# Performance work log

Hardware: AMD Instinct MI355X
Metric: run time of the kernel (lower is better)

Reference implementation:

```python
import jax, jax.numpy as jnp
import numpy as np

N = 100000   # nodes
E = 25000    # hyperedges
NNZ = 2000000
IN_CH = 64
HEADS = 8
OUT_CH = 8
HO = HEADS * OUT_CH  # 64


def setup_inputs() -> dict:
    key = jax.random.key(0)
    k1, k2, k3, k4, k5 = jax.random.split(key, 5)
    X = jax.random.normal(k1, (N, IN_CH), dtype=jnp.float32)
    vertex = jax.random.randint(k2, (NNZ,), 0, N, dtype=jnp.int64 if jax.config.jax_enable_x64 else jnp.int32)
    edges = jax.random.randint(k3, (NNZ,), 0, E, dtype=jnp.int64 if jax.config.jax_enable_x64 else jnp.int32)
    homo = jax.random.uniform(k4, (E,), dtype=jnp.float32) + 0.1  # positive per-hyperedge scalar
    # nn.Linear(in, heads*out, bias=False): store as [in, heads*out] for X @ W
    W = jax.random.normal(k5, (IN_CH, HO), dtype=jnp.float32) * (1.0 / np.sqrt(IN_CH))
    return {"X": X, "W": W, "homo": homo, "vertex": vertex, "edges": edges}


def reference(X, W, homo, vertex, edges):
    n = X.shape[0]
    e = homo.shape[0]
    Xp = X @ W                                   # [N, H*O]
    Xve = Xp[vertex]                             # [nnz, H*O] gather node->incidence
    # first_aggregate = 'mean': vertex features -> hyperedge features
    Xe_sum = jax.ops.segment_sum(Xve, edges, num_segments=e)
    cnt = jax.ops.segment_sum(jnp.ones((Xve.shape[0],), Xve.dtype), edges, num_segments=e)
    Xe = Xe_sum / jnp.maximum(cnt, 1.0)[:, None]  # [E, H*O]
    Xev = Xe[edges]                              # [nnz, H*O] gather edge->incidence
    he = homo[edges]                             # [nnz]
    att_sum = jax.ops.segment_sum(he, vertex, num_segments=n)[vertex]  # [nnz]
    att = he / att_sum                           # [nnz] (homo > 0 so sums > 0 at incident slots)
    att_Xev = att[:, None] * Xev                 # fused version of att.mm(ones).mul(Xev)
    # second_aggregate = 'sum': hyperedge features -> node features
    Xv = jax.ops.segment_sum(att_Xev, vertex, num_segments=n)  # [N, H*O]
    out = Xp + Xv
    # use_norm: row-l2 normalize with DETACHED norm (scale is a constant wrt grad)
    rownorm = jax.lax.stop_gradient(jnp.linalg.norm(out, axis=1, keepdims=True))
    scale = jnp.where(rownorm > 0, 1.0 / jnp.maximum(rownorm, 1e-30), 0.0)
    return out * scale
```

## Files before the change

### kernel.cpp

```cpp
#include <hip/hip_runtime.h>
#include <hip/hip_bf16.h>


#define SE_LOG 6
#define SV_LOG 8
#define MAXB   2048
#define CH     8192

typedef __attribute__((ext_vector_type(8))) short bf16x8;
typedef __attribute__((ext_vector_type(4))) float f32x4;

__device__ __forceinline__ float bf2f(unsigned short u) {
    union { unsigned int i; float f; } x;
    x.i = ((unsigned int)u) << 16;
    return x.f;
}

__device__ __forceinline__ float bflo(unsigned int u) {
    union { unsigned int i; float f; } x;
    x.i = u << 16;
    return x.f;
}

__device__ __forceinline__ float bfhi(unsigned int u) {
    union { unsigned int i; float f; } x;
    x.i = u & 0xffff0000u;
    return x.f;
}

__device__ __forceinline__ unsigned short f2bf(float f) {
    union { unsigned int i; float ff; } x;
    x.ff = f;
    unsigned int r = x.i + 0x7fff + ((x.i >> 16) & 1);
    return (unsigned short)(r >> 16);
}

__device__ __forceinline__ float loadF(const void* p, size_t i, int bf16mode) {
    return bf16mode ? bf2f(((const unsigned short*)p)[i]) : ((const float*)p)[i];
}

__device__ __forceinline__ int loadI(const void* p, size_t i, int i64mode) {
    return i64mode ? ((const int*)p)[2 * i] : ((const int*)p)[i];
}

__global__ void sniff_kernel(const void* X, const void* vtx, int* flags) {
    if (threadIdx.x != 0 || blockIdx.x != 0) return;
    const unsigned short* u = (const unsigned short*)X;
    int sane = 0;
    for (int i = 0; i < 64; ++i) {
        unsigned short lo = u[2 * i];
        int e = (lo >> 7) & 0xFF;
        if (e >= 110 && e <= 137) ++sane;
    }
    flags[0] = (sane >= 32) ? 1 : 0;
    const int* w = (const int*)vtx;
    int zeros = 0;
    for (int i = 0; i < 64; ++i)
        if (w[2 * i + 1] == 0) ++zeros;
    flags[1] = (zeros >= 32) ? 1 : 0;
}

__global__ void homof_kernel(const void* __restrict__ homo,
                             const int* __restrict__ flags,
                             float* __restrict__ homof, int E) {
    int i = blockIdx.x * blockDim.x + threadIdx.x;
    if (i < E) homof[i] = loadF(homo, i, flags[0]);
}

__global__ __launch_bounds__(256)
void gemm_mfma_kernel(const unsigned short* __restrict__ X,
                      const unsigned short* __restrict__ W,
                      const int* __restrict__ flags,
                      unsigned short* __restrict__ Xpb, int N) {
    if (flags[0] == 0) return;
    __shared__ float Ld[4][16 * 68];
    int tid  = threadIdx.x;
    int lane = tid & 63, w = tid >> 6;
    int quad = lane >> 4, c16 = lane & 15;
    bf16x8 bfrag[4][2];
#pragma unroll
    for (int t = 0; t < 4; ++t)
#pragma unroll
        for (int s = 0; s < 2; ++s)
#pragma unroll
            for (int j = 0; j < 8; ++j)
                bfrag[t][s][j] = (short)W[(s * 32 + quad * 8 + j) * 64 + t * 16 + c16];

    int tiles = (N + 15) >> 4;
    int wid = blockIdx.x * 4 + w;
    int nw  = gridDim.x * 4;
    int lr = lane >> 2, seg = lane & 3;
    for (int tile = wid; tile < tiles; tile += nw) {
        int r0 = tile * 16;
        int rA = r0 + c16; if (rA > N - 1) rA = N - 1;
        bf16x8 a0 = *(const bf16x8*)(X + (size_t)rA * 64 + quad * 8);
        bf16x8 a1 = *(const bf16x8*)(X + (size_t)rA * 64 + 32 + quad * 8);
#pragma unroll
        for (int t = 0; t < 4; ++t) {
            f32x4 z = {0.f, 0.f, 0.f, 0.f};
            z = __builtin_amdgcn_mfma_f32_16x16x32_bf16(a0, bfrag[t][0], z, 0, 0, 0);
            z = __builtin_amdgcn_mfma_f32_16x16x32_bf16(a1, bfrag[t][1], z, 0, 0, 0);
#pragma unroll
            for (int i = 0; i < 4; ++i)
                Ld[w][(quad * 4 + i) * 68 + t * 16 + c16] = z[i];
        }
        int r = r0 + lr;
        if (r < N) {
            const float* src = &Ld[w][lr * 68 + seg * 16];
            unsigned int p[8];
#pragma unroll
            for (int i = 0; i < 8; ++i)
                p[i] = (unsigned)f2bf(src[2 * i]) | ((unsigned)f2bf(src[2 * i + 1]) << 16);
            uint4* dst = (uint4*)(Xpb + (size_t)r * 64 + seg * 16);
            dst[0] = make_uint4(p[0], p[1], p[2], p[3]);
            dst[1] = make_uint4(p[4], p[5], p[6], p[7]);
        }
    }
}

__global__ __launch_bounds__(256)
void gemm_f32_kernel(const void* __restrict__ X, const void* __restrict__ W,
                     const int* __restrict__ flags,
                     unsigned short* __restrict__ Xpb, int N) {
    if (flags[0] == 1) return;
    __shared__ float Ws[64 * 64];
    __shared__ float Xs[16][64];
    int tid = threadIdx.x;
    for (int j = tid; j < 4096; j += 256) Ws[j] = ((const float*)W)[j];
    __syncthreads();
    int lane = tid & 63, w = tid >> 6;
    int wid = (blockIdx.x * 256 + tid) >> 6;
    int nw  = (gridDim.x * 256) >> 6;
    for (int r0 = wid * 4; r0 < N; r0 += nw * 4) {
        if (r0 + 4 <= N) {
            float acc0 = 0.f, acc1 = 0.f, acc2 = 0.f, acc3 = 0.f;
#pragma unroll
            for (int j = 0; j < 4; ++j)
                Xs[w * 4 + j][lane] = ((const float*)X)[(size_t)(r0 + j) * 64 + lane];
#pragma unroll
            for (int k4 = 0; k4 < 16; ++k4) {
                float4 x0 = *(const float4*)&Xs[w * 4 + 0][k4 * 4];
                float4 x1 = *(const float4*)&Xs[w * 4 + 1][k4 * 4];
                float4 x2 = *(const float4*)&Xs[w * 4 + 2][k4 * 4];
                float4 x3 = *(const float4*)&Xs[w * 4 + 3][k4 * 4];
#pragma unroll
                for (int kk = 0; kk < 4; ++kk) {
                    float wv = Ws[(k4 * 4 + kk) * 64 + lane];
                    acc0 = fmaf((&x0.x)[kk], wv, acc0);
                    acc1 = fmaf((&x1.x)[kk], wv, acc1);
                    acc2 = fmaf((&x2.x)[kk], wv, acc2);
                    acc3 = fmaf((&x3.x)[kk], wv, acc3);
                }
            }
            float a[4] = {acc0, acc1, acc2, acc3};
#pragma unroll
            for (int j = 0; j < 4; ++j)
                Xpb[(size_t)(r0 + j) * 64 + lane] = f2bf(a[j]);
        } else {
            for (int r = r0; r < N; ++r) {
                Xs[w * 4][lane] = ((const float*)X)[(size_t)r * 64 + lane];
                float acc = 0.f;
                for (int k = 0; k < 64; ++k)
                    acc = fmaf(Xs[w * 4][k], Ws[k * 64 + lane], acc);
                Xpb[(size_t)r * 64 + lane] = f2bf(acc);
            }
        }
    }
}

__global__ __launch_bounds__(1024)
void bhist_kernel(const void* __restrict__ edges, const void* __restrict__ vertex,
                  const int* __restrict__ flags, int* __restrict__ btot,
                  int* __restrict__ slabc, int sstride,
                  int nnz, int NBE, int NBV, int GC) {
    __shared__ int cnt[MAXB];
    int blk  = blockIdx.x;
    int side = (blk >= GC) ? 1 : 0;
    int b    = side ? blk - GC : blk;
    const void* keys = side ? vertex : edges;
    int sblog = side ? SV_LOG : SE_LOG;
    int nb    = side ? NBV : NBE;
    int bas   = side ? NBE : 0;
    int tid = threadIdx.x;
    for (int j = tid; j < nb; j += 1024) cnt[j] = 0;
    __syncthreads();
    int imode = flags[1];
    int c0 = b * CH, c1 = min(nnz, c0 + CH);
    for (int i = c0 + tid; i < c1; i += 1024)
        atomicAdd(&cnt[loadI(keys, i, imode) >> sblog], 1);
    __syncthreads();
    for (int j = tid; j < nb; j += 1024) {
        int c = cnt[j];
        slabc[(size_t)blk * sstride + j] = c;
        if (c) atomicAdd(&btot[bas + j], c);
    }
}

__global__ void bscan_kernel(const int* __restrict__ btot, int* __restrict__ bbase,
                             int* __restrict__ bcur, int NBT) {
    __shared__ int wsum[16];
    __shared__ int carry_s;
    int tid = threadIdx.x, lane = tid & 63, w = tid >> 6;
    if (tid == 0) carry_s = 0;
    __syncthreads();
    for (int base = 0; base < NBT; base += 1024) {
        int i = base + tid;
        int x = (i < NBT) ? btot[i] : 0;
        int s = x;
#pragma unroll
        for (int d = 1; d < 64; d <<= 1) {
            int t = __shfl_up(s, d, 64);
            if (lane >= d) s += t;
        }
        if (lane == 63) wsum[w] = s;
        __syncthreads();
        if (w == 0 && lane < 16) {
            int v = wsum[lane];
#pragma unroll
            for (int d = 1; d < 16; d <<= 1) {
                int t = __shfl_up(v, d, 64);
                if (lane >= d) v += t;
            }
            wsum[lane] = v;
        }
        __syncthreads();
        int carry = carry_s;
        int excl  = carry + (w > 0 ? wsum[w - 1] : 0) + s - x;
        if (i < NBT) { bbase[i] = excl; bcur[i] = excl; }
        __syncthreads();
        if (tid == 1023) carry_s = carry + wsum[15];
        __syncthreads();
    }
    if (tid == 0) bbase[NBT] = carry_s;
}

__global__ __launch_bounds__(1024)
void bscatter_kernel(const void* __restrict__ edges, const void* __restrict__ vertex,
                     const int* __restrict__ flags, int* __restrict__ bcur,
                     const int* __restrict__ slabc, int sstride,
                     int* __restrict__ buck, int nnz, int NBE, int NBV, int GC,
                     int bitsN, int bitsE) {
    __shared__ int cnt[MAXB];
    __shared__ int gb[MAXB];
    int blk  = blockIdx.x;
    int side = (blk >= GC) ? 1 : 0;
    int b    = side ? blk - GC : blk;
    const void* keys = side ? vertex : edges;
    const void* pay  = side ? edges  : vertex;
    int sblog = side ? SV_LOG : SE_LOG;
    int psh   = side ? bitsE : bitsN;
    int nb    = side ? NBV : NBE;
    int bas   = side ? NBE : 0;
    int tid = threadIdx.x;
    for (int j = tid; j < nb; j += 1024) {
        int c = slabc[(size_t)blk * sstride + j];
        gb[j]  = c ? atomicAdd(&bcur[bas + j], c) : 0;
        cnt[j] = 0;
    }
    __syncthreads();
    int imode = flags[1];
    int c0 = b * CH, c1 = min(nnz, c0 + CH);
    int lmask = (1 << sblog) - 1;
    for (int i = c0 + tid; i < c1; i += 1024) {
        int k   = loadI(keys, i, imode);
        int bkt = k >> sblog;
        int r   = atomicAdd(&cnt[bkt], 1);
        buck[gb[bkt] + r] = ((k & lmask) << psh) | loadI(pay, i, imode);
    }
}

__global__ __launch_bounds__(1024)
void bfinal_kernel(const int* __restrict__ buck, const int* __restrict__ bbase,
                   const float* __restrict__ homof,
                   int* __restrict__ off, int* __restrict__ dest,
                   float* __restrict__ hs,
                   int NBE, int NBV, int E, int N, int bitsN, int bitsE) {
    __shared__ int cnt[1 << SV_LOG];
    __shared__ int sexc[1 << SV_LOG];
    __shared__ float hsum[1 << SV_LOG];
    __shared__ int wsum[16];
    int g    = blockIdx.x;
    int side = (g >= NBE) ? 1 : 0;
    int b    = side ? g - NBE : g;
    int sblog = side ? SV_LOG : SE_LOG;
    int psh   = side ? bitsE : bitsN;
    int pmask = (1 << psh) - 1;
    int nside = side ? N : E;
    int bin0  = b << sblog;
    int nbins = min(1 << sblog, nside - bin0);
    int goff0 = (side ? E : 0) + bin0;
    int s0 = bbase[g], s1 = bbase[g + 1], size = s1 - s0;
    int tid = threadIdx.x, lane = tid & 63, w = tid >> 6;
    for (int j = tid; j < nbins; j += 1024) { cnt[j] = 0; hsum[j] = 0.f; }
    __syncthreads();
    for (int j = tid; j < size; j += 1024)
        atomicAdd(&cnt[buck[s0 + j] >> psh], 1);
    __syncthreads();
    {
        int x = (tid < nbins) ? cnt[tid] : 0;
        int s = x;
#pragma unroll
        for (int d = 1; d < 64; d <<= 1) {
            int t = __shfl_up(s, d, 64);
            if (lane >= d) s += t;
        }
        if (lane == 63) wsum[w] = s;
        __syncthreads();
        if (w == 0 && lane < 16) {
            int v = wsum[lane];
#pragma unroll
            for (int d = 1; d < 16; d <<= 1) {
                int t = __shfl_up(v, d, 64);
                if (lane >= d) v += t;
            }
            wsum[lane] = v;
        }
        __syncthreads();
        int excl = s - x + (w > 0 ? wsum[w - 1] : 0);
        if (tid < nbins) { sexc[tid] = excl; off[goff0 + tid] = s0 + excl; }
    }
    if (side == 1 && b == NBV - 1 && tid == 0) off[E + N] = s1;
    __syncthreads();
    for (int j = tid; j < nbins; j += 1024) cnt[j] = sexc[j];
    __syncthreads();
    if (side == 1) {
        for (int j = tid; j < size; j += 1024) {
            int p  = buck[s0 + j];
            int lb = p >> psh;
            int r  = atomicAdd(&cnt[lb], 1);
            int e  = p & pmask;
            dest[s0 + r] = e;
            atomicAdd(&hsum[lb], homof[e]);
        }
        __syncthreads();
        for (int j = tid; j < nbins; j += 1024) hs[bin0 + j] = hsum[j];
    } else {
        for (int j = tid; j < size; j += 1024) {
            int p = buck[s0 + j];
            int r = atomicAdd(&cnt[p >> psh], 1);
            dest[s0 + r] = p & pmask;
        }
    }
}

__global__ void hist_atomic_kernel(const void* __restrict__ edges,
                                   const void* __restrict__ vertex,
                                   const int* __restrict__ flags,
                                   int* __restrict__ tot, int E, int nnz) {
    int i = blockIdx.x * blockDim.x + threadIdx.x;
    if (i >= nnz) return;
    int imode = flags[1];
    atomicAdd(&tot[loadI(edges, i, imode)], 1);
    atomicAdd(&tot[E + loadI(vertex, i, imode)], 1);
}

__global__ void scan_part_kernel(const int* __restrict__ tot, int* __restrict__ part, int M) {
    int g = blockIdx.x, tid = threadIdx.x;
    int base = g * 2048;
    int sum = 0;
    for (int j = tid; j < 2048; j += 256) {
        int i = base + j;
        sum += (i < M) ? tot[i] : 0;
    }
#pragma unroll
    for (int d = 32; d >= 1; d >>= 1) sum += __shfl_xor(sum, d, 64);
    __shared__ int wsums[4];
    int lane = tid & 63, w = tid >> 6;
    if (lane == 0) wsums[w] = sum;
    __syncthreads();
    if (tid == 0) part[g] = wsums[0] + wsums[1] + wsums[2] + wsums[3];
}

__global__ void scan_root_kernel(int* __restrict__ part, int G,
                                 int* __restrict__ off, int M) {
    int tid = threadIdx.x, lane = tid & 63, w = tid >> 6;
    int x = (tid < G) ? part[tid] : 0;
    int s = x;
#pragma unroll
    for (int d = 1; d < 64; d <<= 1) {
        int t = __shfl_up(s, d, 64);
        if (lane >= d) s += t;
    }
    __shared__ int ws[16];
    if (lane == 63) ws[w] = s;
    __syncthreads();
    if (w == 0 && lane < 16) {
        int v = ws[lane];
#pragma unroll
        for (int d = 1; d < 16; d <<= 1) {
            int t = __shfl_up(v, d, 64);
            if (lane >= d) v += t;
        }
        ws[lane] = v;
    }
    __syncthreads();
    int excl = s - x + (w > 0 ? ws[w - 1] : 0);
    if (tid < G) part[tid] = excl;
    if (tid == 1023) off[M] = ws[15];
}

__global__ void scan_apply_kernel(int* __restrict__ tot, const int* __restrict__ part,
                                  int* __restrict__ off, int M) {
    int g = blockIdx.x, tid = threadIdx.x, lane = tid & 63, w = tid >> 6;
    int base = g * 2048 + tid * 8;
    int e[8]; int s = 0;
#pragma unroll
    for (int j = 0; j < 8; ++j) {
        int i = base + j;
        e[j] = (i < M) ? tot[i] : 0;
        s += e[j];
    }
    int si = s;
#pragma unroll
    for (int d = 1; d < 64; d <<= 1) {
        int t = __shfl_up(si, d, 64);
        if (lane >= d) si += t;
    }
    __shared__ int wsum[4];
    if (lane == 63) wsum[w] = si;
    __syncthreads();
    int wbase = 0;
    for (int ww = 0; ww < w; ++ww) wbase += wsum[ww];
    int run = part[g] + wbase + si - s;
#pragma unroll
    for (int j = 0; j < 8; ++j) {
        int i = base + j;
        if (i < M) off[i] = run;
        run += e[j];
    }
}

__global__ void copy_kernel(const int* __restrict__ src, int* __restrict__ dst, int n) {
    int i = blockIdx.x * blockDim.x + threadIdx.x;
    if (i < n) dst[i] = src[i];
}

__global__ void scatter_atomic_kernel(const void* __restrict__ edges,
                                      const void* __restrict__ vertex,
                                      const int* __restrict__ flags,
                                      int* __restrict__ cur, int* __restrict__ dest,
                                      int E, int nnz) {
    int i = blockIdx.x * blockDim.x + threadIdx.x;
    if (i >= nnz) return;
    int imode = flags[1];
    int e = loadI(edges, i, imode);
    int v = loadI(vertex, i, imode);
    dest[atomicAdd(&cur[e], 1)]     = v;
    dest[atomicAdd(&cur[E + v], 1)] = e;
}

__global__ void hs_fallback_kernel(const int* __restrict__ off,
                                   const int* __restrict__ sorted,
                                   const float* __restrict__ homof,
                                   float* __restrict__ hs, int E, int N) {
    int v = blockIdx.x * blockDim.x + threadIdx.x;
    if (v >= N) return;
    int s = off[E + v], e = off[E + v + 1];
    float t = 0.f;
    for (int j = s; j < e; ++j) t += homof[sorted[j]];
    hs[v] = t;
}

__global__ void edge_mean_kernel(const unsigned short* __restrict__ Xpb,
                                 const int* __restrict__ off,
                                 const int* __restrict__ sorted,
                                 const float* __restrict__ homof,
                                 unsigned short* __restrict__ Ye, int E) {
    int wid  = (blockIdx.x * blockDim.x + threadIdx.x) >> 6;
    int lane = threadIdx.x & 63;
    if (wid >= E) return;
    int g = lane >> 4, c = lane & 15;
    unsigned co = (unsigned)c << 3;
    int start = off[wid], end = off[wid + 1];
    float a0 = 0.f, a1 = 0.f, a2 = 0.f, a3 = 0.f;
    const char* Xb = (const char*)Xpb;
    int j = start + g;
    for (; j + 12 < end; j += 16) {
        int v0 = sorted[j];
        int v1 = sorted[j + 4];
        int v2 = sorted[j + 8];
        int v3 = sorted[j + 12];
        uint2 u0 = *(const uint2*)(Xb + (((unsigned)v0 << 7) + co));
        uint2 u1 = *(const uint2*)(Xb + (((unsigned)v1 << 7) + co));
        uint2 u2 = *(const uint2*)(Xb + (((unsigned)v2 << 7) + co));
        uint2 u3 = *(const uint2*)(Xb + (((unsigned)v3 << 7) + co));
        a0 += (bflo(u0.x) + bflo(u1.x)) + (bflo(u2.x) + bflo(u3.x));
        a1 += (bfhi(u0.x) + bfhi(u1.x)) + (bfhi(u2.x) + bfhi(u3.x));
        a2 += (bflo(u0.y) + bflo(u1.y)) + (bflo(u2.y) + bflo(u3.y));
        a3 += (bfhi(u0.y) + bfhi(u1.y)) + (bfhi(u2.y) + bfhi(u3.y));
    }
    for (; j < end; j += 4) {
        int v = sorted[j];
        uint2 u = *(const uint2*)(Xb + (((unsigned)v << 7) + co));
        a0 += bflo(u.x); a1 += bfhi(u.x);
        a2 += bflo(u.y); a3 += bfhi(u.y);
    }
    a0 += __shfl_xor(a0, 16, 64); a0 += __shfl_xor(a0, 32, 64);
    a1 += __shfl_xor(a1, 16, 64); a1 += __shfl_xor(a1, 32, 64);
    a2 += __shfl_xor(a2, 16, 64); a2 += __shfl_xor(a2, 32, 64);
    a3 += __shfl_xor(a3, 16, 64); a3 += __shfl_xor(a3, 32, 64);
    if (g == 0) {
        float inv = homof[wid] / fmaxf((float)(end - start), 1.f);
        unsigned p0 = (unsigned)f2bf(a0 * inv) | ((unsigned)f2bf(a1 * inv) << 16);
        unsigned p1 = (unsigned)f2bf(a2 * inv) | ((unsigned)f2bf(a3 * inv) << 16);
        *(uint2*)((char*)Ye + (((unsigned)wid << 7) + co)) = make_uint2(p0, p1);
    }
}

__global__ void vertex_out_kernel(const unsigned short* __restrict__ Xpb,
                                  const unsigned short* __restrict__ Ye,
                                  const int* __restrict__ off,
                                  const int* __restrict__ sorted,
                                  const float* __restrict__ hs,
                                  float* __restrict__ out, int E, int N) {
    int wv   = (blockIdx.x * blockDim.x + threadIdx.x) >> 6;
    int lane = threadIdx.x & 63;
    int g = lane >> 3, c = lane & 7;
    int vid = wv * 8 + g;
    if (vid >= N) return;
    unsigned co = (unsigned)c << 4;
    int start = off[E + vid], end = off[E + vid + 1];
    float a0 = 0.f, a1 = 0.f, a2 = 0.f, a3 = 0.f;
    float a4 = 0.f, a5 = 0.f, a6 = 0.f, a7 = 0.f;
    const char* Yb = (const char*)Ye;
    int j = start;
    for (; j + 3 < end; j += 4) {
        int e0 = sorted[j], e1 = sorted[j + 1], e2 = sorted[j + 2], e3 = sorted[j + 3];
        uint4 u0 = *(const uint4*)(Yb + (((unsigned)e0 << 7) + co));
        uint4 u1 = *(const uint4*)(Yb + (((unsigned)e1 << 7) + co));
        uint4 u2 = *(const uint4*)(Yb + (((unsigned)e2 << 7) + co));
        uint4 u3 = *(const uint4*)(Yb + (((unsigned)e3 << 7) + co));
        a0 += (bflo(u0.x) + bflo(u1.x)) + (bflo(u2.x) + bflo(u3.x));
        a1 += (bfhi(u0.x) + bfhi(u1.x)) + (bfhi(u2.x) + bfhi(u3.x));
        a2 += (bflo(u0.y) + bflo(u1.y)) + (bflo(u2.y) + bflo(u3.y));
        a3 += (bfhi(u0.y) + bfhi(u1.y)) + (bfhi(u2.y) + bfhi(u3.y));
        a4 += (bflo(u0.z) + bflo(u1.z)) + (bflo(u2.z) + bflo(u3.z));
        a5 += (bfhi(u0.z) + bfhi(u1.z)) + (bfhi(u2.z) + bfhi(u3.z));
        a6 += (bflo(u0.w) + bflo(u1.w)) + (bflo(u2.w) + bflo(u3.w));
        a7 += (bfhi(u0.w) + bfhi(u1.w)) + (bfhi(u2.w) + bfhi(u3.w));
    }
    for (; j < end; ++j) {
        int e = sorted[j];
        uint4 u = *(const uint4*)(Yb + (((unsigned)e << 7) + co));
        a0 += bflo(u.x); a1 += bfhi(u.x);
        a2 += bflo(u.y); a3 += bfhi(u.y);
        a4 += bflo(u.z); a5 += bfhi(u.z);
        a6 += bflo(u.w); a7 += bfhi(u.w);
    }
    float hsv = hs[vid];
    float inv = (hsv > 0.f) ? 1.f / hsv : 0.f;
    uint4 xu = *(const uint4*)((const char*)Xpb + (((unsigned)vid << 7) + co));
    float r0 = bflo(xu.x) + a0 * inv, r1 = bfhi(xu.x) + a1 * inv;
    float r2 = bflo(xu.y) + a2 * inv, r3 = bfhi(xu.y) + a3 * inv;
    float r4 = bflo(xu.z) + a4 * inv, r5 = bfhi(xu.z) + a5 * inv;
    float r6 = bflo(xu.w) + a6 * inv, r7 = bfhi(xu.w) + a7 * inv;
    float ss = ((r0 * r0 + r1 * r1) + (r2 * r2 + r3 * r3)) +
               ((r4 * r4 + r5 * r5) + (r6 * r6 + r7 * r7));
    ss += __shfl_xor(ss, 1, 64);
    ss += __shfl_xor(ss, 2, 64);
    ss += __shfl_xor(ss, 4, 64);
    float rn    = sqrtf(ss);
    float scale = (rn > 0.f) ? 1.f / fmaxf(rn, 1e-30f) : 0.f;
    char* ob = (char*)out + (((unsigned)vid << 8) + (co << 1));
    *(float4*)ob        = make_float4(r0 * scale, r1 * scale, r2 * scale, r3 * scale);
    *(float4*)(ob + 16) = make_float4(r4 * scale, r5 * scale, r6 * scale, r7 * scale);
}

static inline int ceil_bits(int n) {
    int v = n - 1;
    if (v < 1) v = 1;
    int b = 0;
    while ((1 << b) <= v) ++b;
    return b;
}

extern "C" void kernel_launch(void* const* d_in, const int* in_sizes, int n_in,
                              void* d_out, int out_size, void* d_ws, size_t ws_size,
                              hipStream_t stream) {
    const void* X      = d_in[0];
    const void* W      = d_in[1];
    const void* homo   = d_in[2];
    const void* vertex = d_in[3];
    const void* edges  = d_in[4];
    float* out = (float*)d_out;

    const int N   = in_sizes[0] / 64;
    const int E   = in_sizes[2];
    const int NNZ = in_sizes[3];
    const int M   = E + N;

    const int NBE = (E + (1 << SE_LOG) - 1) >> SE_LOG;
    const int NBV = (N + (1 << SV_LOG) - 1) >> SV_LOG;
    const int NBT = NBE + NBV;
    const int GC  = (NNZ + CH - 1) / CH;
    const int SST = (NBE > NBV ? NBE : NBV);
    const int bitsN = ceil_bits(N);
    const int bitsE = ceil_bits(E);
    const int G   = (M + 2047) / 2048;

    char*  ws = (char*)d_ws;
    size_t o  = 0;
    auto alloc = [&](size_t bytes) -> void* {
        void* p = ws + o;
        o += (bytes + 255) & ~(size_t)255;
        return p;
    };
    int*            flags = (int*)alloc(2 * 4);
    int*            off   = (int*)alloc((size_t)(M + 1) * 4);
    int*            bbase = (int*)alloc((size_t)(NBT + 1) * 4);
    int*            bcur  = (int*)alloc((size_t)NBT * 4);
    int*            btot  = (int*)alloc((size_t)NBT * 4);
    float*          homof = (float*)alloc((size_t)E * 4);
    float*          hs    = (float*)alloc((size_t)N * 4);
    int*            buck  = (int*)alloc((size_t)2 * NNZ * 4);
    int*            sorted= (int*)alloc((size_t)2 * NNZ * 4);
    unsigned short* Xpb   = (unsigned short*)alloc((size_t)N * 64 * 2);
    unsigned short* Ye    = (unsigned short*)alloc((size_t)E * 64 * 2);
    int*            slabc = (int*)alloc((size_t)2 * GC * SST * 4);
    size_t o_common = o;
    bool fast = (o <= ws_size) && NBE <= MAXB && NBV <= MAXB &&
                (SE_LOG + bitsN <= 32) && (SV_LOG + bitsE <= 32) && G <= 1024;
    (void)n_in; (void)out_size;

    sniff_kernel<<<1, 64, 0, stream>>>(X, vertex, flags);
    homof_kernel<<<(E + 255) / 256, 256, 0, stream>>>(homo, flags, homof, E);
    gemm_mfma_kernel<<<1024, 256, 0, stream>>>((const unsigned short*)X,
                                               (const unsigned short*)W,
                                               flags, Xpb, N);
    gemm_f32_kernel<<<512, 256, 0, stream>>>(X, W, flags, Xpb, N);

    if (fast) {
        hipMemsetAsync(btot, 0, (size_t)NBT * 4, stream);
        bhist_kernel<<<2 * GC, 1024, 0, stream>>>(edges, vertex, flags, btot,
                                                  slabc, SST, NNZ, NBE, NBV, GC);
        bscan_kernel<<<1, 1024, 0, stream>>>(btot, bbase, bcur, NBT);
        bscatter_kernel<<<2 * GC, 1024, 0, stream>>>(edges, vertex, flags, bcur,
                                                     slabc, SST, buck, NNZ,
                                                     NBE, NBV, GC, bitsN, bitsE);
        bfinal_kernel<<<NBT, 1024, 0, stream>>>(buck, bbase, homof, off, sorted,
                                                hs, NBE, NBV, E, N, bitsN, bitsE);
    } else {
        o = o_common;
        int* tot  = (int*)alloc((size_t)M * 4);
        int* part = (int*)alloc((size_t)(G + 1) * 4);
        int* cur  = (int*)alloc((size_t)M * 4);
        hipMemsetAsync(tot, 0, (size_t)M * 4, stream);
        int nb = (NNZ + 255) / 256;
        hist_atomic_kernel<<<nb, 256, 0, stream>>>(edges, vertex, flags, tot, E, NNZ);
        scan_part_kernel<<<G, 256, 0, stream>>>(tot, part, M);
        scan_root_kernel<<<1, 1024, 0, stream>>>(part, G, off, M);
        scan_apply_kernel<<<G, 256, 0, stream>>>(tot, part, off, M);
        copy_kernel<<<(M + 255) / 256, 256, 0, stream>>>(off, cur, M);
        scatter_atomic_kernel<<<nb, 256, 0, stream>>>(edges, vertex, flags, cur, sorted, E, NNZ);
        hs_fallback_kernel<<<(N + 255) / 256, 256, 0, stream>>>(off, sorted, homof, hs, E, N);
    }

    edge_mean_kernel<<<(E + 3) / 4, 256, 0, stream>>>(Xpb, off, sorted, homof, Ye, E);
    int vwaves  = (N + 7) / 8;
    int vblocks = (vwaves * 64 + 255) / 256;
    vertex_out_kernel<<<vblocks, 256, 0, stream>>>(Xpb, Ye, off, sorted,
                                                   hs, out, E, N);
}
```

Before: 254.0 us.

## Fuse bucket finalize with edge-mean and vertex-output aggregation using LDS lists

Histogram and scatter now handle both the edge and vertex sides in a single pass over the inputs, so edges and vertex are each read once instead of twice. The per-bucket finalize is merged with the edge-mean and vertex-output computations: the sorted neighbour lists are kept in LDS, and the global sorted array and offset array are no longer written out and read back. A spill path to global memory covers buckets larger than the LDS capacity. In exchange, the fused blocks use a lot of shared memory, which lowers occupancy, and each bucket is handled by a single block, which lowers parallelism in the gather phases.

New measurement: 245.7 us. 1.03x faster.

```diff
diff --git a/kernel.cpp b/kernel.cpp
--- a/kernel.cpp
+++ b/kernel.cpp
@@ -4,8 +4,8 @@
 
 #define SE_LOG 6
 #define SV_LOG 8
-#define MAXB   2048
-#define CH     8192
+#define CH     4096
+#define CAPB   12288
 
 typedef __attribute__((ext_vector_type(8))) short bf16x8;
 typedef __attribute__((ext_vector_type(4))) float f32x4;
@@ -169,30 +169,26 @@
 }
 
 __global__ __launch_bounds__(1024)
-void bhist_kernel(const void* __restrict__ edges, const void* __restrict__ vertex,
-                  const int* __restrict__ flags, int* __restrict__ btot,
-                  int* __restrict__ slabc, int sstride,
-                  int nnz, int NBE, int NBV, int GC) {
-    __shared__ int cnt[MAXB];
-    int blk  = blockIdx.x;
-    int side = (blk >= GC) ? 1 : 0;
-    int b    = side ? blk - GC : blk;
-    const void* keys = side ? vertex : edges;
-    int sblog = side ? SV_LOG : SE_LOG;
-    int nb    = side ? NBV : NBE;
-    int bas   = side ? NBE : 0;
-    int tid = threadIdx.x;
-    for (int j = tid; j < nb; j += 1024) cnt[j] = 0;
+void bhist2_kernel(const void* __restrict__ edges, const void* __restrict__ vertex,
+                   const int* __restrict__ flags, int* __restrict__ btot,
+                   int* __restrict__ slabc, int nnz, int NBE, int NBT) {
+    __shared__ int cnt[2048];
+    int tid = threadIdx.x, b = blockIdx.x;
+    for (int j = tid; j < NBT; j += 1024) cnt[j] = 0;
     __syncthreads();
     int imode = flags[1];
     int c0 = b * CH, c1 = min(nnz, c0 + CH);
-    for (int i = c0 + tid; i < c1; i += 1024)
-        atomicAdd(&cnt[loadI(keys, i, imode) >> sblog], 1);
-    __syncthreads();
-    for (int j = tid; j < nb; j += 1024) {
+    for (int i = c0 + tid; i < c1; i += 1024) {
+        int e = loadI(edges, i, imode);
+        int v = loadI(vertex, i, imode);
+        atomicAdd(&cnt[e >> SE_LOG], 1);
+        atomicAdd(&cnt[NBE + (v >> SV_LOG)], 1);
+    }
+    __syncthreads();
+    for (int j = tid; j < NBT; j += 1024) {
         int c = cnt[j];
-        slabc[(size_t)blk * sstride + j] = c;
-        if (c) atomicAdd(&btot[bas + j], c);
+        slabc[(size_t)b * NBT + j] = c;
+        if (c) atomicAdd(&btot[j], c);
     }
 }
 
@@ -235,66 +231,152 @@
 }
 
 __global__ __launch_bounds__(1024)
-void bscatter_kernel(const void* __restrict__ edges, const void* __restrict__ vertex,
-                     const int* __restrict__ flags, int* __restrict__ bcur,
-                     const int* __restrict__ slabc, int sstride,
-                     int* __restrict__ buck, int nnz, int NBE, int NBV, int GC,
-                     int bitsN, int bitsE) {
-    __shared__ int cnt[MAXB];
-    __shared__ int gb[MAXB];
-    int blk  = blockIdx.x;
-    int side = (blk >= GC) ? 1 : 0;
-    int b    = side ? blk - GC : blk;
-    const void* keys = side ? vertex : edges;
-    const void* pay  = side ? edges  : vertex;
-    int sblog = side ? SV_LOG : SE_LOG;
-    int psh   = side ? bitsE : bitsN;
-    int nb    = side ? NBV : NBE;
-    int bas   = side ? NBE : 0;
-    int tid = threadIdx.x;
-    for (int j = tid; j < nb; j += 1024) {
-        int c = slabc[(size_t)blk * sstride + j];
-        gb[j]  = c ? atomicAdd(&bcur[bas + j], c) : 0;
+void bscatter2_kernel(const void* __restrict__ edges, const void* __restrict__ vertex,
+                      const int* __restrict__ flags, int* __restrict__ bcur,
+                      const int* __restrict__ slabc, int* __restrict__ buck,
+                      int nnz, int NBE, int NBT, int bitsN, int bitsE) {
+    __shared__ int cnt[2048];
+    __shared__ int gb[2048];
+    int tid = threadIdx.x, b = blockIdx.x;
+    for (int j = tid; j < NBT; j += 1024) {
+        int c = slabc[(size_t)b * NBT + j];
+        gb[j]  = c ? atomicAdd(&bcur[j], c) : 0;
         cnt[j] = 0;
     }
     __syncthreads();
     int imode = flags[1];
     int c0 = b * CH, c1 = min(nnz, c0 + CH);
-    int lmask = (1 << sblog) - 1;
     for (int i = c0 + tid; i < c1; i += 1024) {
-        int k   = loadI(keys, i, imode);
-        int bkt = k >> sblog;
-        int r   = atomicAdd(&cnt[bkt], 1);
-        buck[gb[bkt] + r] = ((k & lmask) << psh) | loadI(pay, i, imode);
+        int e = loadI(edges, i, imode);
+        int v = loadI(vertex, i, imode);
+        int be = e >> SE_LOG;
+        int r  = atomicAdd(&cnt[be], 1);
+        buck[gb[be] + r] = ((e & ((1 << SE_LOG) - 1)) << bitsN) | v;
+        int bv = NBE + (v >> SV_LOG);
+        int r2 = atomicAdd(&cnt[bv], 1);
+        buck[gb[bv] + r2] = ((v & ((1 << SV_LOG) - 1)) << bitsE) | e;
     }
 }
 
 __global__ __launch_bounds__(1024)
-void bfinal_kernel(const int* __restrict__ buck, const int* __restrict__ bbase,
-                   const float* __restrict__ homof,
-                   int* __restrict__ off, int* __restrict__ dest,
-                   float* __restrict__ hs,
-                   int NBE, int NBV, int E, int N, int bitsN, int bitsE) {
+void bfe_kernel(const int* __restrict__ buck, const int* __restrict__ bbase,
+                const float* __restrict__ homof, int* __restrict__ spill,
+                const unsigned short* __restrict__ Xpb,
+                unsigned short* __restrict__ Ye, int E, int bitsN) {
+    __shared__ int list[CAPB];
+    __shared__ int cnt[1 << SE_LOG];
+    __shared__ int sexc[1 << SE_LOG];
+    __shared__ int wsum[16];
+    int g = blockIdx.x;
+    int bin0 = g << SE_LOG;
+    int nbins = min(1 << SE_LOG, E - bin0);
+    int s0 = bbase[g], s1 = bbase[g + 1], size = s1 - s0;
+    int tid = threadIdx.x, lane = tid & 63, w = tid >> 6;
+    bool sp = (size > CAPB);
+    int pmask = (1 << bitsN) - 1;
+    for (int j = tid; j < nbins; j += 1024) cnt[j] = 0;
+    __syncthreads();
+    for (int j = tid; j < size; j += 1024)
+        atomicAdd(&cnt[buck[s0 + j] >> bitsN], 1);
+    __syncthreads();
+    {
+        int x = (tid < nbins) ? cnt[tid] : 0;
+        int s = x;
+#pragma unroll
+        for (int d = 1; d < 64; d <<= 1) {
+            int t = __shfl_up(s, d, 64);
+            if (lane >= d) s += t;
+        }
+        if (lane == 63) wsum[w] = s;
+        __syncthreads();
+        if (w == 0 && lane < 16) {
+            int v = wsum[lane];
+#pragma unroll
+            for (int d = 1; d < 16; d <<= 1) {
+                int t = __shfl_up(v, d, 64);
+                if (lane >= d) v += t;
+            }
+            wsum[lane] = v;
+        }
+        __syncthreads();
+        int excl = s - x + (w > 0 ? wsum[w - 1] : 0);
+        if (tid < nbins) sexc[tid] = excl;
+    }
+    __syncthreads();
+    if (tid < nbins) cnt[tid] = sexc[tid];
+    __syncthreads();
+    for (int j = tid; j < size; j += 1024) {
+        int p  = buck[s0 + j];
+        int lb = p >> bitsN;
+        int r  = atomicAdd(&cnt[lb], 1);
+        int v  = p & pmask;
+        if (sp) spill[s0 + r] = v; else list[r] = v;
+    }
+    __syncthreads();
+    int grp = (w << 2) | (lane >> 4);
+    int c = lane & 15;
+    unsigned co = (unsigned)c << 3;
+    if (grp < nbins) {
+        int start = sexc[grp], end = cnt[grp];
+        const char* Xb = (const char*)Xpb;
+        float a0 = 0.f, a1 = 0.f, a2 = 0.f, a3 = 0.f;
+        int j = start;
+        if (!sp) {
+            for (; j + 3 < end; j += 4) {
+                int v0 = list[j], v1 = list[j + 1], v2 = list[j + 2], v3 = list[j + 3];
+                uint2 u0 = *(const uint2*)(Xb + (((unsigned)v0 << 7) + co));
+                uint2 u1 = *(const uint2*)(Xb + (((unsigned)v1 << 7) + co));
+                uint2 u2 = *(const uint2*)(Xb + (((unsigned)v2 << 7) + co));
+                uint2 u3 = *(const uint2*)(Xb + (((unsigned)v3 << 7) + co));
+                a0 += (bflo(u0.x) + bflo(u1.x)) + (bflo(u2.x) + bflo(u3.x));
+                a1 += (bfhi(u0.x) + bfhi(u1.x)) + (bfhi(u2.x) + bfhi(u3.x));
+                a2 += (bflo(u0.y) + bflo(u1.y)) + (bflo(u2.y) + bflo(u3.y));
+                a3 += (bfhi(u0.y) + bfhi(u1.y)) + (bfhi(u2.y) + bfhi(u3.y));
+            }
+            for (; j < end; ++j) {
+                int v = list[j];
+                uint2 u = *(const uint2*)(Xb + (((unsigned)v << 7) + co));
+                a0 += bflo(u.x); a1 += bfhi(u.x);
+                a2 += bflo(u.y); a3 += bfhi(u.y);
+            }
+        } else {
+            for (; j < end; ++j) {
+                int v = spill[s0 + j];
+                uint2 u = *(const uint2*)(Xb + (((unsigned)v << 7) + co));
+                a0 += bflo(u.x); a1 += bfhi(u.x);
+                a2 += bflo(u.y); a3 += bfhi(u.y);
+            }
+        }
+        int e = bin0 + grp;
+        float inv = homof[e] / fmaxf((float)(end - start), 1.f);
+        unsigned p0 = (unsigned)f2bf(a0 * inv) | ((unsigned)f2bf(a1 * inv) << 16);
+        unsigned p1 = (unsigned)f2bf(a2 * inv) | ((unsigned)f2bf(a3 * inv) << 16);
+        *(uint2*)((char*)Ye + (((unsigned)e << 7) + co)) = make_uint2(p0, p1);
+    }
+}
+
+__global__ __launch_bounds__(1024)
+void bfv_kernel(const int* __restrict__ buck, const int* __restrict__ bbase,
+                const float* __restrict__ homof, int* __restrict__ spill,
+                const unsigned short* __restrict__ Xpb,
+                const unsigned short* __restrict__ Ye,
+                float* __restrict__ out, int N, int NBE, int bitsE) {
+    __shared__ int list[CAPB];
     __shared__ int cnt[1 << SV_LOG];
     __shared__ int sexc[1 << SV_LOG];
     __shared__ float hsum[1 << SV_LOG];
     __shared__ int wsum[16];
-    int g    = blockIdx.x;
-    int side = (g >= NBE) ? 1 : 0;
-    int b    = side ? g - NBE : g;
-    int sblog = side ? SV_LOG : SE_LOG;
-    int psh   = side ? bitsE : bitsN;
-    int pmask = (1 << psh) - 1;
-    int nside = side ? N : E;
-    int bin0  = b << sblog;
-    int nbins = min(1 << sblog, nside - bin0);
-    int goff0 = (side ? E : 0) + bin0;
-    int s0 = bbase[g], s1 = bbase[g + 1], size = s1 - s0;
+    int bv = blockIdx.x;
+    int bin0 = bv << SV_LOG;
+    int nbins = min(1 << SV_LOG, N - bin0);
+    int s0 = bbase[NBE + bv], s1 = bbase[NBE + bv + 1], size = s1 - s0;
     int tid = threadIdx.x, lane = tid & 63, w = tid >> 6;
+    bool sp = (size > CAPB);
+    int pmask = (1 << bitsE) - 1;
     for (int j = tid; j < nbins; j += 1024) { cnt[j] = 0; hsum[j] = 0.f; }
     __syncthreads();
     for (int j = tid; j < size; j += 1024)
-        atomicAdd(&cnt[buck[s0 + j] >> psh], 1);
+        atomicAdd(&cnt[buck[s0 + j] >> bitsE], 1);
     __syncthreads();
     {
         int x = (tid < nbins) ? cnt[tid] : 0;
@@ -317,29 +399,81 @@
         }
         __syncthreads();
         int excl = s - x + (w > 0 ? wsum[w - 1] : 0);
-        if (tid < nbins) { sexc[tid] = excl; off[goff0 + tid] = s0 + excl; }
-    }
-    if (side == 1 && b == NBV - 1 && tid == 0) off[E + N] = s1;
-    __syncthreads();
-    for (int j = tid; j < nbins; j += 1024) cnt[j] = sexc[j];
-    __syncthreads();
-    if (side == 1) {
-        for (int j = tid; j < size; j += 1024) {
-            int p  = buck[s0 + j];
-            int lb = p >> psh;
-            int r  = atomicAdd(&cnt[lb], 1);
-            int e  = p & pmask;
-            dest[s0 + r] = e;
-            atomicAdd(&hsum[lb], homof[e]);
-        }
-        __syncthreads();
-        for (int j = tid; j < nbins; j += 1024) hs[bin0 + j] = hsum[j];
-    } else {
-        for (int j = tid; j < size; j += 1024) {
-            int p = buck[s0 + j];
-            int r = atomicAdd(&cnt[p >> psh], 1);
-            dest[s0 + r] = p & pmask;
-        }
+        if (tid < nbins) sexc[tid] = excl;
+    }
+    __syncthreads();
+    if (tid < nbins) cnt[tid] = sexc[tid];
+    __syncthreads();
+    for (int j = tid; j < size; j += 1024) {
+        int p  = buck[s0 + j];
+        int lb = p >> bitsE;
+        int r  = atomicAdd(&cnt[lb], 1);
+        int e  = p & pmask;
+        if (sp) spill[s0 + r] = e; else list[r] = e;
+        atomicAdd(&hsum[lb], homof[e]);
+    }
+    __syncthreads();
+    int grp = (w << 3) | (lane >> 3);
+    int c = lane & 7;
+    unsigned co = (unsigned)c << 4;
+    const char* Yb = (const char*)Ye;
+    for (int vl = grp; vl < nbins; vl += 128) {
+        int start = sexc[vl], end = cnt[vl];
+        float a0 = 0.f, a1 = 0.f, a2 = 0.f, a3 = 0.f;
+        float a4 = 0.f, a5 = 0.f, a6 = 0.f, a7 = 0.f;
+        int j = start;
+        if (!sp) {
+            for (; j + 3 < end; j += 4) {
+                int e0 = list[j], e1 = list[j + 1], e2 = list[j + 2], e3 = list[j + 3];
+                uint4 u0 = *(const uint4*)(Yb + (((unsigned)e0 << 7) + co));
+                uint4 u1 = *(const uint4*)(Yb + (((unsigned)e1 << 7) + co));
+                uint4 u2 = *(const uint4*)(Yb + (((unsigned)e2 << 7) + co));
+                uint4 u3 = *(const uint4*)(Yb + (((unsigned)e3 << 7) + co));
+                a0 += (bflo(u0.x) + bflo(u1.x)) + (bflo(u2.x) + bflo(u3.x));
+                a1 += (bfhi(u0.x) + bfhi(u1.x)) + (bfhi(u2.x) + bfhi(u3.x));
+                a2 += (bflo(u0.y) + bflo(u1.y)) + (bflo(u2.y) + bflo(u3.y));
+                a3 += (bfhi(u0.y) + bfhi(u1.y)) + (bfhi(u2.y) + bfhi(u3.y));
+                a4 += (bflo(u0.z) + bflo(u1.z)) + (bflo(u2.z) + bflo(u3.z));
+                a5 += (bfhi(u0.z) + bfhi(u1.z)) + (bfhi(u2.z) + bfhi(u3.z));
+                a6 += (bflo(u0.w) + bflo(u1.w)) + (bflo(u2.w) + bflo(u3.w));
+                a7 += (bfhi(u0.w) + bfhi(u1.w)) + (bfhi(u2.w) + bfhi(u3.w));
+            }
+            for (; j < end; ++j) {
+                int e = list[j];
+                uint4 u = *(const uint4*)(Yb + (((unsigned)e << 7) + co));
+                a0 += bflo(u.x); a1 += bfhi(u.x);
+                a2 += bflo(u.y); a3 += bfhi(u.y);
+                a4 += bflo(u.z); a5 += bfhi(u.z);
+                a6 += bflo(u.w); a7 += bfhi(u.w);
+            }
+        } else {
+            for (; j < end; ++j) {
+                int e = spill[s0 + j];
+                uint4 u = *(const uint4*)(Yb + (((unsigned)e << 7) + co));
+                a0 += bflo(u.x); a1 += bfhi(u.x);
+                a2 += bflo(u.y); a3 += bfhi(u.y);
+                a4 += bflo(u.z); a5 += bfhi(u.z);
+                a6 += bflo(u.w); a7 += bfhi(u.w);
+            }
+        }
+        int vid = bin0 + vl;
+        float hsv = hsum[vl];
+        float inv = (hsv > 0.f) ? 1.f / hsv : 0.f;
+        uint4 xu = *(const uint4*)((const char*)Xpb + (((unsigned)vid << 7) + co));
+        float r0 = bflo(xu.x) + a0 * inv, r1 = bfhi(xu.x) + a1 * inv;
+        float r2 = bflo(xu.y) + a2 * inv, r3 = bfhi(xu.y) + a3 * inv;
+        float r4 = bflo(xu.z) + a4 * inv, r5 = bfhi(xu.z) + a5 * inv;
+        float r6 = bflo(xu.w) + a6 * inv, r7 = bfhi(xu.w) + a7 * inv;
+        float ss = ((r0 * r0 + r1 * r1) + (r2 * r2 + r3 * r3)) +
+                   ((r4 * r4 + r5 * r5) + (r6 * r6 + r7 * r7));
+        ss += __shfl_xor(ss, 1, 64);
+        ss += __shfl_xor(ss, 2, 64);
+        ss += __shfl_xor(ss, 4, 64);
+        float rn    = sqrtf(ss);
+        float scale = (rn > 0.f) ? 1.f / fmaxf(rn, 1e-30f) : 0.f;
+        char* ob = (char*)out + (((unsigned)vid << 8) + (co << 1));
+        *(float4*)ob        = make_float4(r0 * scale, r1 * scale, r2 * scale, r3 * scale);
+        *(float4*)(ob + 16) = make_float4(r4 * scale, r5 * scale, r6 * scale, r7 * scale);
     }
 }
 
@@ -474,22 +608,7 @@
     int start = off[wid], end = off[wid + 1];
     float a0 = 0.f, a1 = 0.f, a2 = 0.f, a3 = 0.f;
     const char* Xb = (const char*)Xpb;
-    int j = start + g;
-    for (; j + 12 < end; j += 16) {
-        int v0 = sorted[j];
-        int v1 = sorted[j + 4];
-        int v2 = sorted[j + 8];
-        int v3 = sorted[j + 12];
-        uint2 u0 = *(const uint2*)(Xb + (((unsigned)v0 << 7) + co));
-        uint2 u1 = *(const uint2*)(Xb + (((unsigned)v1 << 7) + co));
-        uint2 u2 = *(const uint2*)(Xb + (((unsigned)v2 << 7) + co));
-        uint2 u3 = *(const uint2*)(Xb + (((unsigned)v3 << 7) + co));
-        a0 += (bflo(u0.x) + bflo(u1.x)) + (bflo(u2.x) + bflo(u3.x));
-        a1 += (bfhi(u0.x) + bfhi(u1.x)) + (bfhi(u2.x) + bfhi(u3.x));
-        a2 += (bflo(u0.y) + bflo(u1.y)) + (bflo(u2.y) + bflo(u3.y));
-        a3 += (bfhi(u0.y) + bfhi(u1.y)) + (bfhi(u2.y) + bfhi(u3.y));
-    }
-    for (; j < end; j += 4) {
+    for (int j = start + g; j < end; j += 4) {
         int v = sorted[j];
         uint2 u = *(const uint2*)(Xb + (((unsigned)v << 7) + co));
         a0 += bflo(u.x); a1 += bfhi(u.x);
@@ -523,23 +642,7 @@
     float a0 = 0.f, a1 = 0.f, a2 = 0.f, a3 = 0.f;
     float a4 = 0.f, a5 = 0.f, a6 = 0.f, a7 = 0.f;
     const char* Yb = (const char*)Ye;
-    int j = start;
-    for (; j + 3 < end; j += 4) {
-        int e0 = sorted[j], e1 = sorted[j + 1], e2 = sorted[j + 2], e3 = sorted[j + 3];
-        uint4 u0 = *(const uint4*)(Yb + (((unsigned)e0 << 7) + co));
-        uint4 u1 = *(const uint4*)(Yb + (((unsigned)e1 << 7) + co));
-        uint4 u2 = *(const uint4*)(Yb + (((unsigned)e2 << 7) + co));
-        uint4 u3 = *(const uint4*)(Yb + (((unsigned)e3 << 7) + co));
-        a0 += (bflo(u0.x) + bflo(u1.x)) + (bflo(u2.x) + bflo(u3.x));
-        a1 += (bfhi(u0.x) + bfhi(u1.x)) + (bfhi(u2.x) + bfhi(u3.x));
-        a2 += (bflo(u0.y) + bflo(u1.y)) + (bflo(u2.y) + bflo(u3.y));
-        a3 += (bfhi(u0.y) + bfhi(u1.y)) + (bfhi(u2.y) + bfhi(u3.y));
-        a4 += (bflo(u0.z) + bflo(u1.z)) + (bflo(u2.z) + bflo(u3.z));
-        a5 += (bfhi(u0.z) + bfhi(u1.z)) + (bfhi(u2.z) + bfhi(u3.z));
-        a6 += (bflo(u0.w) + bflo(u1.w)) + (bflo(u2.w) + bflo(u3.w));
-        a7 += (bfhi(u0.w) + bfhi(u1.w)) + (bfhi(u2.w) + bfhi(u3.w));
-    }
-    for (; j < end; ++j) {
+    for (int j = start; j < end; ++j) {
         int e = sorted[j];
         uint4 u = *(const uint4*)(Yb + (((unsigned)e << 7) + co));
         a0 += bflo(u.x); a1 += bfhi(u.x);
@@ -593,7 +696,6 @@
     const int NBV = (N + (1 << SV_LOG) - 1) >> SV_LOG;
     const int NBT = NBE + NBV;
     const int GC  = (NNZ + CH - 1) / CH;
-    const int SST = (NBE > NBV ? NBE : NBV);
     const int bitsN = ceil_bits(N);
     const int bitsE = ceil_bits(E);
     const int G   = (M + 2047) / 2048;
@@ -606,20 +708,18 @@
         return p;
     };
     int*            flags = (int*)alloc(2 * 4);
-    int*            off   = (int*)alloc((size_t)(M + 1) * 4);
     int*            bbase = (int*)alloc((size_t)(NBT + 1) * 4);
     int*            bcur  = (int*)alloc((size_t)NBT * 4);
     int*            btot  = (int*)alloc((size_t)NBT * 4);
     float*          homof = (float*)alloc((size_t)E * 4);
-    float*          hs    = (float*)alloc((size_t)N * 4);
     int*            buck  = (int*)alloc((size_t)2 * NNZ * 4);
-    int*            sorted= (int*)alloc((size_t)2 * NNZ * 4);
+    int*            spill = (int*)alloc((size_t)2 * NNZ * 4);
     unsigned short* Xpb   = (unsigned short*)alloc((size_t)N * 64 * 2);
     unsigned short* Ye    = (unsigned short*)alloc((size_t)E * 64 * 2);
-    int*            slabc = (int*)alloc((size_t)2 * GC * SST * 4);
+    int*            slabc = (int*)alloc((size_t)GC * NBT * 4);
     size_t o_common = o;
-    bool fast = (o <= ws_size) && NBE <= MAXB && NBV <= MAXB &&
-                (SE_LOG + bitsN <= 32) && (SV_LOG + bitsE <= 32) && G <= 1024;
+    bool fast = (o <= ws_size) && NBT <= 2048 &&
+                (SE_LOG + bitsN <= 31) && (SV_LOG + bitsE <= 31) && G <= 1024;
     (void)n_in; (void)out_size;
 
     sniff_kernel<<<1, 64, 0, stream>>>(X, vertex, flags);
@@ -631,19 +731,24 @@
 
     if (fast) {
         hipMemsetAsync(btot, 0, (size_t)NBT * 4, stream);
-        bhist_kernel<<<2 * GC, 1024, 0, stream>>>(edges, vertex, flags, btot,
-                                                  slabc, SST, NNZ, NBE, NBV, GC);
+        bhist2_kernel<<<GC, 1024, 0, stream>>>(edges, vertex, flags, btot,
+                                               slabc, NNZ, NBE, NBT);
         bscan_kernel<<<1, 1024, 0, stream>>>(btot, bbase, bcur, NBT);
-        bscatter_kernel<<<2 * GC, 1024, 0, stream>>>(edges, vertex, flags, bcur,
-                                                     slabc, SST, buck, NNZ,
-                                                     NBE, NBV, GC, bitsN, bitsE);
-        bfinal_kernel<<<NBT, 1024, 0, stream>>>(buck, bbase, homof, off, sorted,
-                                                hs, NBE, NBV, E, N, bitsN, bitsE);
+        bscatter2_kernel<<<GC, 1024, 0, stream>>>(edges, vertex, flags, bcur,
+                                                  slabc, buck, NNZ, NBE, NBT,
+                                                  bitsN, bitsE);
+        bfe_kernel<<<NBE, 1024, 0, stream>>>(buck, bbase, homof, spill,
+                                             Xpb, Ye, E, bitsN);
+        bfv_kernel<<<NBV, 1024, 0, stream>>>(buck, bbase, homof, spill,
+                                             Xpb, Ye, out, N, NBE, bitsE);
     } else {
         o = o_common;
+        int* off  = (int*)alloc((size_t)(M + 1) * 4);
+        float* hs = (float*)alloc((size_t)N * 4);
         int* tot  = (int*)alloc((size_t)M * 4);
         int* part = (int*)alloc((size_t)(G + 1) * 4);
         int* cur  = (int*)alloc((size_t)M * 4);
+        int* sorted = spill;
         hipMemsetAsync(tot, 0, (size_t)M * 4, stream);
         int nb = (NNZ + 255) / 256;
         hist_atomic_kernel<<<nb, 256, 0, stream>>>(edges, vertex, flags, tot, E, NNZ);
@@ -653,11 +758,9 @@
         copy_kernel<<<(M + 255) / 256, 256, 0, stream>>>(off, cur, M);
         scatter_atomic_kernel<<<nb, 256, 0, stream>>>(edges, vertex, flags, cur, sorted, E, NNZ);
         hs_fallback_kernel<<<(N + 255) / 256, 256, 0, stream>>>(off, sorted, homof, hs, E, N);
-    }
-
-    edge_mean_kernel<<<(E + 3) / 4, 256, 0, stream>>>(Xpb, off, sorted, homof, Ye, E);
-    int vwaves  = (N + 7) / 8;
-    int vblocks = (vwaves * 64 + 255) / 256;
-    vertex_out_kernel<<<vblocks, 256, 0, stream>>>(Xpb, Ye, off, sorted,
-                                                   hs, out, E, N);
-}
+        edge_mean_kernel<<<(E + 3) / 4, 256, 0, stream>>>(Xpb, off, sorted, homof, Ye, E);
+        int vwaves  = (N + 7) / 8;
+        int vblocks = (vwaves * 64 + 255) / 256;
+        vertex_out_kernel<<<vblocks, 256, 0, stream>>>(Xpb, Ye, off, sorted, hs, out, E, N);
+    }
+}
```
